# Kernel optimization log

Hardware: AMD Instinct MI355X
Metric: run time of the kernel (lower is better)

## Reference

```python
import jax, jax.numpy as jnp
import numpy as np

N_NODES = 20000
N_EDGES = 640000
NODE_IN = 128
EDGE_IN = 64
HID = 128
OUT = 128
LOG2 = float(np.log(2.0))


def ssp(x):
    # DGL ShiftedSoftplus: softplus(x) - log(2)
    return jax.nn.softplus(x) - LOG2


def cfconv(x, e, src, dst,
           nW, nb, eW1, eb1, eW2, eb2, oW, ob):
    hv = x @ nW + nb                                  # [N, HID]
    he = ssp(ssp(e @ eW1 + eb1) @ eW2 + eb2)          # [E, HID]
    msg = hv[src] * he                                # gather + filter
    agg = jax.ops.segment_sum(msg, dst, num_segments=N_NODES)
    return ssp(agg @ oW + ob)


def setup_inputs() -> dict:
    key = jax.random.key(0)
    ks = jax.random.split(key, 20)
    def w(k, shape, fan_in):
        return jax.random.normal(k, shape, dtype=jnp.float32) * (1.0 / np.sqrt(fan_in))
    inp = {
        "node_inputs": jax.random.normal(ks[0], (N_NODES, NODE_IN), dtype=jnp.float32),
        "edge_inputs": jax.random.normal(ks[1], (N_EDGES, EDGE_IN), dtype=jnp.float32),
        "src": jax.random.randint(ks[2], (N_EDGES,), 0, N_NODES, dtype=jnp.int32),
        "dst": jax.random.randint(ks[3], (N_EDGES,), 0, N_NODES, dtype=jnp.int32),
        # conv1 params
        "n1_W": w(ks[4], (NODE_IN, HID), NODE_IN), "n1_b": jnp.zeros((HID,), jnp.float32),
        "e1_W1": w(ks[5], (EDGE_IN, HID), EDGE_IN), "e1_b1": jnp.zeros((HID,), jnp.float32),
        "e1_W2": w(ks[6], (HID, HID), HID), "e1_b2": jnp.zeros((HID,), jnp.float32),
        "o1_W": w(ks[7], (HID, HID), HID), "o1_b": jnp.zeros((HID,), jnp.float32),
        # conv2 params
        "n2_W": w(ks[8], (HID, HID), HID), "n2_b": jnp.zeros((HID,), jnp.float32),
        "e2_W1": w(ks[9], (EDGE_IN, HID), EDGE_IN), "e2_b1": jnp.zeros((HID,), jnp.float32),
        "e2_W2": w(ks[10], (HID, HID), HID), "e2_b2": jnp.zeros((HID,), jnp.float32),
        "o2_W": w(ks[11], (HID, OUT), HID), "o2_b": jnp.zeros((OUT,), jnp.float32),
    }
    return inp


def reference(node_inputs, edge_inputs, src, dst,
              n1_W, n1_b, e1_W1, e1_b1, e1_W2, e1_b2, o1_W, o1_b,
              n2_W, n2_b, e2_W1, e2_b1, e2_W2, e2_b2, o2_W, o2_b):
    h = cfconv(node_inputs, edge_inputs, src, dst,
               n1_W, n1_b, e1_W1, e1_b1, e1_W2, e1_b2, o1_W, o1_b)
    h = jnp.tanh(h)
    # dropout(p) is identity in eval mode
    h = cfconv(h, edge_inputs, src, dst,
               n2_W, n2_b, e2_W1, e2_b1, e2_W2, e2_b2, o2_W, o2_b)
    return jnp.tanh(h)
```

## Files before the change

kernel.cpp:

```cpp
#include <hip/hip_runtime.h>
#include <hip/hip_bf16.h>
#include <math.h>

typedef __bf16 bf16x8 __attribute__((ext_vector_type(8)));
typedef float f32x4 __attribute__((ext_vector_type(4)));

#define LOG2F 0.6931471805599453f
#define PK1 72
#define PK2 136

__device__ __forceinline__ float sspf(float x) {
    float t = __expf(-fabsf(x));
    return fmaxf(x, 0.0f) + __logf(1.0f + t) - LOG2F;
}

__device__ __forceinline__ unsigned short f2bf(float f) {
    union { float f; unsigned u; } v; v.f = f;
    unsigned r = v.u + 0x7FFF + ((v.u >> 16) & 1);
    return (unsigned short)(r >> 16);
}

__device__ __forceinline__ unsigned short f2bf_fast(float f) {
    __bf16 h = (__bf16)f;
    return __builtin_bit_cast(unsigned short, h);
}

template<int ACT>
__global__ void node_gemm(const float* __restrict__ X, const float* __restrict__ W,
                          const float* __restrict__ b, float* __restrict__ Y, int N) {
    __shared__ float xs[2][128];
    const int tid = threadIdx.x;
    const int r = tid >> 7;
    const int c = tid & 127;
    const int row = blockIdx.x * 2 + r;
    if (row < N) xs[r][c] = X[(size_t)row * 128 + c];
    __syncthreads();
    if (row >= N) return;
    float acc = b[c];
#pragma unroll 8
    for (int k = 0; k < 128; ++k)
        acc = fmaf(xs[r][k], W[k * 128 + c], acc);
    if (ACT) acc = tanhf(sspf(acc));
    Y[(size_t)row * 128 + c] = acc;
}

__global__ void convert_wT(const float* __restrict__ W, unsigned short* __restrict__ O,
                           int K, int PK) {
    int idx = blockIdx.x * 256 + threadIdx.x;
    if (idx >= 128 * PK) return;
    int n = idx / PK, k = idx - n * PK;
    O[idx] = (k < K) ? f2bf(W[k * 128 + n]) : (unsigned short)0;
}

__global__ __launch_bounds__(256) void edge_mfma(
    const float* __restrict__ E, const int* __restrict__ src, const int* __restrict__ dst,
    const float* __restrict__ HV,
    const unsigned short* __restrict__ W1T, const float* __restrict__ b1,
    const unsigned short* __restrict__ W2T, const float* __restrict__ b2,
    float* __restrict__ AGG, int nE)
{
    __shared__ unsigned short sE[64 * PK1];
    __shared__ unsigned short sT1[64 * PK2];
    __shared__ int sSrc[64], sDst[64];

    const int tid = threadIdx.x;
    const int e0 = blockIdx.x * 64;

    {
        const int r = tid >> 2;
        const int c0 = (tid & 3) * 16;
        unsigned short* drow = &sE[r * PK1 + c0];
        if (e0 + r < nE) {
            const float4* s4 = (const float4*)&E[(size_t)(e0 + r) * 64 + c0];
#pragma unroll
            for (int j = 0; j < 4; ++j) {
                float4 v = s4[j];
                drow[j * 4 + 0] = f2bf_fast(v.x); drow[j * 4 + 1] = f2bf_fast(v.y);
                drow[j * 4 + 2] = f2bf_fast(v.z); drow[j * 4 + 3] = f2bf_fast(v.w);
            }
        } else {
#pragma unroll
            for (int j = 0; j < 16; ++j) drow[j] = 0;
        }
        if (tid < 64) {
            int e = e0 + tid;
            sSrc[tid] = (e < nE) ? src[e] : 0;
            sDst[tid] = (e < nE) ? dst[e] : 0;
        }
    }
    __syncthreads();

    const int w  = tid >> 6;
    const int l  = tid & 63;
    const int cb = w * 32;
    const int lr = l & 15;
    const int lk = (l >> 4) * 8;

    bf16x8 B1[2][2];
#pragma unroll
    for (int nt = 0; nt < 2; ++nt)
#pragma unroll
        for (int kt = 0; kt < 2; ++kt)
            B1[nt][kt] = *(const bf16x8*)&W1T[(cb + nt * 16 + lr) * PK1 + kt * 32 + lk];

    const float bb1[2] = { b1[cb + lr], b1[cb + 16 + lr] };
    const float bb2[2] = { b2[cb + lr], b2[cb + 16 + lr] };

    f32x4 acc1[4][2];
#pragma unroll
    for (int mt = 0; mt < 4; ++mt)
#pragma unroll
        for (int nt = 0; nt < 2; ++nt)
            acc1[mt][nt] = (f32x4){bb1[nt], bb1[nt], bb1[nt], bb1[nt]};
#pragma unroll
    for (int kt = 0; kt < 2; ++kt)
#pragma unroll
        for (int mt = 0; mt < 4; ++mt) {
            bf16x8 A = *(const bf16x8*)&sE[(mt * 16 + lr) * PK1 + kt * 32 + lk];
#pragma unroll
            for (int nt = 0; nt < 2; ++nt)
                acc1[mt][nt] = __builtin_amdgcn_mfma_f32_16x16x32_bf16(A, B1[nt][kt], acc1[mt][nt], 0, 0, 0);
        }

#pragma unroll
    for (int mt = 0; mt < 4; ++mt)
#pragma unroll
        for (int nt = 0; nt < 2; ++nt) {
            const int col = cb + nt * 16 + lr;
#pragma unroll
            for (int r = 0; r < 4; ++r) {
                const int row = mt * 16 + (l >> 4) * 4 + r;
                sT1[row * PK2 + col] = f2bf_fast(sspf(acc1[mt][nt][r]));
            }
        }
    __syncthreads();

    bf16x8 B2[2][4];
#pragma unroll
    for (int nt = 0; nt < 2; ++nt)
#pragma unroll
        for (int kt = 0; kt < 4; ++kt)
            B2[nt][kt] = *(const bf16x8*)&W2T[(cb + nt * 16 + lr) * PK2 + kt * 32 + lk];

    f32x4 acc2[4][2];
#pragma unroll
    for (int mt = 0; mt < 4; ++mt)
#pragma unroll
        for (int nt = 0; nt < 2; ++nt)
            acc2[mt][nt] = (f32x4){bb2[nt], bb2[nt], bb2[nt], bb2[nt]};
#pragma unroll
    for (int kt = 0; kt < 4; ++kt)
#pragma unroll
        for (int mt = 0; mt < 4; ++mt) {
            bf16x8 A = *(const bf16x8*)&sT1[(mt * 16 + lr) * PK2 + kt * 32 + lk];
#pragma unroll
            for (int nt = 0; nt < 2; ++nt)
                acc2[mt][nt] = __builtin_amdgcn_mfma_f32_16x16x32_bf16(A, B2[nt][kt], acc2[mt][nt], 0, 0, 0);
        }

#pragma unroll
    for (int mt = 0; mt < 4; ++mt)
#pragma unroll
        for (int nt = 0; nt < 2; ++nt) {
            const int col = cb + nt * 16 + lr;
#pragma unroll
            for (int r = 0; r < 4; ++r) {
                const int row = mt * 16 + (l >> 4) * 4 + r;
                if (e0 + row < nE) {
                    const float he = sspf(acc2[mt][nt][r]);
                    const int s = sSrc[row], d = sDst[row];
                    const float m = HV[(size_t)s * 128 + col] * he;
                    atomicAdd(&AGG[(size_t)d * 128 + col], m);
                }
            }
        }
}

extern "C" void kernel_launch(void* const* d_in, const int* in_sizes, int n_in,
                              void* d_out, int out_size, void* d_ws, size_t ws_size,
                              hipStream_t stream) {
    const float* x    = (const float*)d_in[0];
    const float* e    = (const float*)d_in[1];
    const int*   src  = (const int*)  d_in[2];
    const int*   dst  = (const int*)  d_in[3];
    const float* n1W  = (const float*)d_in[4];
    const float* n1b  = (const float*)d_in[5];
    const float* e1W1 = (const float*)d_in[6];
    const float* e1b1 = (const float*)d_in[7];
    const float* e1W2 = (const float*)d_in[8];
    const float* e1b2 = (const float*)d_in[9];
    const float* o1W  = (const float*)d_in[10];
    const float* o1b  = (const float*)d_in[11];
    const float* n2W  = (const float*)d_in[12];
    const float* n2b  = (const float*)d_in[13];
    const float* e2W1 = (const float*)d_in[14];
    const float* e2b1 = (const float*)d_in[15];
    const float* e2W2 = (const float*)d_in[16];
    const float* e2b2 = (const float*)d_in[17];
    const float* o2W  = (const float*)d_in[18];
    const float* o2b  = (const float*)d_in[19];

    const int N = in_sizes[0] / 128;
    const int E = in_sizes[2];
    float* out = (float*)d_out;

    char* ws = (char*)d_ws;
    const size_t nbytes = (size_t)N * 128 * sizeof(float);
    float* hv   = (float*)(ws);
    float* agg  = (float*)(ws + nbytes);
    float* hbuf = (float*)(ws + 2 * nbytes);

    const size_t w1t_elems = 128 * PK1;
    const size_t w2t_elems = 128 * PK2;
    const size_t wbytes = 2 * (w1t_elems + w2t_elems) * sizeof(unsigned short);
    unsigned short* wbase;
    if (ws_size >= 3 * nbytes + wbytes) {
        wbase = (unsigned short*)(ws + 3 * nbytes);
    } else {
        wbase = (unsigned short*)d_out;
    }
    unsigned short* w1t_1 = wbase;
    unsigned short* w2t_1 = wbase + w1t_elems;
    unsigned short* w1t_2 = wbase + w1t_elems + w2t_elems;
    unsigned short* w2t_2 = wbase + 2 * w1t_elems + w2t_elems;

    const int nodeBlocks = (N + 1) / 2;
    const int edgeBlocks = (E + 63) / 64;

    convert_wT<<<(128 * PK1 + 255) / 256, 256, 0, stream>>>(e1W1, w1t_1, 64,  PK1);
    convert_wT<<<(128 * PK2 + 255) / 256, 256, 0, stream>>>(e1W2, w2t_1, 128, PK2);
    convert_wT<<<(128 * PK1 + 255) / 256, 256, 0, stream>>>(e2W1, w1t_2, 64,  PK1);
    convert_wT<<<(128 * PK2 + 255) / 256, 256, 0, stream>>>(e2W2, w2t_2, 128, PK2);

    node_gemm<0><<<nodeBlocks, 256, 0, stream>>>(x, n1W, n1b, hv, N);
    hipMemsetAsync(agg, 0, nbytes, stream);
    edge_mfma<<<edgeBlocks, 256, 0, stream>>>(e, src, dst, hv, w1t_1, e1b1, w2t_1, e1b2, agg, E);
    node_gemm<1><<<nodeBlocks, 256, 0, stream>>>(agg, o1W, o1b, hbuf, N);

    node_gemm<0><<<nodeBlocks, 256, 0, stream>>>(hbuf, n2W, n2b, hv, N);
    hipMemsetAsync(agg, 0, nbytes, stream);
    edge_mfma<<<edgeBlocks, 256, 0, stream>>>(e, src, dst, hv, w1t_2, e2b1, w2t_2, e2b2, agg, E);
    node_gemm<1><<<nodeBlocks, 256, 0, stream>>>(agg, o2W, o2b, out, N);
}
```

Measured before the change: 753.2 us.

## Sort edges by destination and coalesce atomics per run of equal dst

```diff
diff --git a/kernel.cpp b/kernel.cpp
--- a/kernel.cpp
+++ b/kernel.cpp
@@ -13,13 +13,11 @@
     float t = __expf(-fabsf(x));
     return fmaxf(x, 0.0f) + __logf(1.0f + t) - LOG2F;
 }
-
 __device__ __forceinline__ unsigned short f2bf(float f) {
     union { float f; unsigned u; } v; v.f = f;
     unsigned r = v.u + 0x7FFF + ((v.u >> 16) & 1);
     return (unsigned short)(r >> 16);
 }
-
 __device__ __forceinline__ unsigned short f2bf_fast(float f) {
     __bf16 h = (__bf16)f;
     return __builtin_bit_cast(unsigned short, h);
@@ -52,60 +50,111 @@
     O[idx] = (k < K) ? f2bf(W[k * 128 + n]) : (unsigned short)0;
 }
 
+__global__ void hist_kernel(const int* __restrict__ dst, int* __restrict__ hist, int E) {
+    int i = blockIdx.x * 256 + threadIdx.x;
+    if (i < E) atomicAdd(&hist[dst[i]], 1);
+}
+__global__ void scan_kernel(const int* __restrict__ hist, int* __restrict__ row_ptr,
+                            int* __restrict__ cursor, int N) {
+    __shared__ int part[1024];
+    const int tid = threadIdx.x;
+    const int chunk = (N + 1023) / 1024;
+    const int lo = min(tid * chunk, N);
+    const int hi = min(lo + chunk, N);
+    int s = 0;
+    for (int i = lo; i < hi; ++i) s += hist[i];
+    part[tid] = s;
+    __syncthreads();
+    if (tid == 0) {
+        int run = 0;
+        for (int i = 0; i < 1024; ++i) { int t = part[i]; part[i] = run; run += t; }
+    }
+    __syncthreads();
+    int run = part[tid];
+    for (int i = lo; i < hi; ++i) { row_ptr[i] = run; cursor[i] = run; run += hist[i]; }
+}
+__global__ void scatter_kernel(const int* __restrict__ dst, int* __restrict__ cursor,
+                               int* __restrict__ perm, int E) {
+    int i = blockIdx.x * 256 + threadIdx.x;
+    if (i < E) { int p = atomicAdd(&cursor[dst[i]], 1); perm[p] = i; }
+}
+__global__ void sort_buckets(const int* __restrict__ row_ptr, const int* __restrict__ hist,
+                             int* __restrict__ perm, int N) {
+    int n = blockIdx.x * 256 + threadIdx.x;
+    if (n >= N) return;
+    const int lo = row_ptr[n], hi = lo + hist[n];
+    for (int i = lo + 1; i < hi; ++i) {
+        int v = perm[i]; int j = i - 1;
+        while (j >= lo && perm[j] > v) { perm[j + 1] = perm[j]; --j; }
+        perm[j + 1] = v;
+    }
+}
+__global__ void permute_sd(const int* __restrict__ perm, const int* __restrict__ src,
+                           const int* __restrict__ dst, int* __restrict__ srcP,
+                           int* __restrict__ dstP, int E) {
+    int i = blockIdx.x * 256 + threadIdx.x;
+    if (i < E) { int e = perm[i]; srcP[i] = src[e]; dstP[i] = dst[e]; }
+}
+__global__ void permute_e(const int* __restrict__ perm, const float* __restrict__ Ef,
+                          unsigned short* __restrict__ Ebf, int nE) {
+    long long idx = (long long)blockIdx.x * 256 + threadIdx.x;
+    if (idx >= (long long)nE * 16) return;
+    int p = (int)(idx >> 4), q = (int)(idx & 15);
+    int e = perm[p];
+    float4 v = *(const float4*)&Ef[(size_t)e * 64 + q * 4];
+    unsigned short* o = &Ebf[(size_t)p * 64 + q * 4];
+    o[0] = f2bf_fast(v.x); o[1] = f2bf_fast(v.y);
+    o[2] = f2bf_fast(v.z); o[3] = f2bf_fast(v.w);
+}
+
+template<int MODE>
 __global__ __launch_bounds__(256) void edge_mfma(
-    const float* __restrict__ E, const int* __restrict__ src, const int* __restrict__ dst,
+    const unsigned short* __restrict__ Ebf, const float* __restrict__ Ef,
+    const int* __restrict__ perm,
+    const int* __restrict__ srcA, const int* __restrict__ dstA,
     const float* __restrict__ HV,
     const unsigned short* __restrict__ W1T, const float* __restrict__ b1,
     const unsigned short* __restrict__ W2T, const float* __restrict__ b2,
     float* __restrict__ AGG, int nE)
 {
-    __shared__ unsigned short sE[64 * PK1];
     __shared__ unsigned short sT1[64 * PK2];
     __shared__ int sSrc[64], sDst[64];
+    __shared__ unsigned short sE[(MODE == 1) ? 64 * PK1 : 4];
 
     const int tid = threadIdx.x;
     const int e0 = blockIdx.x * 64;
 
-    {
-        const int r = tid >> 2;
-        const int c0 = (tid & 3) * 16;
-        unsigned short* drow = &sE[r * PK1 + c0];
-        if (e0 + r < nE) {
-            const float4* s4 = (const float4*)&E[(size_t)(e0 + r) * 64 + c0];
-#pragma unroll
-            for (int j = 0; j < 4; ++j) {
-                float4 v = s4[j];
-                drow[j * 4 + 0] = f2bf_fast(v.x); drow[j * 4 + 1] = f2bf_fast(v.y);
-                drow[j * 4 + 2] = f2bf_fast(v.z); drow[j * 4 + 3] = f2bf_fast(v.w);
-            }
-        } else {
-#pragma unroll
-            for (int j = 0; j < 16; ++j) drow[j] = 0;
-        }
-        if (tid < 64) {
-            int e = e0 + tid;
-            sSrc[tid] = (e < nE) ? src[e] : 0;
-            sDst[tid] = (e < nE) ? dst[e] : 0;
-        }
-    }
-    __syncthreads();
-
-    const int w  = tid >> 6;
-    const int l  = tid & 63;
-    const int cb = w * 32;
-    const int lr = l & 15;
-    const int lk = (l >> 4) * 8;
-
-    bf16x8 B1[2][2];
-#pragma unroll
-    for (int nt = 0; nt < 2; ++nt)
-#pragma unroll
-        for (int kt = 0; kt < 2; ++kt)
-            B1[nt][kt] = *(const bf16x8*)&W1T[(cb + nt * 16 + lr) * PK1 + kt * 32 + lk];
-
+    if (tid < 64) {
+        int gi = min(e0 + tid, nE - 1);
+        sSrc[tid] = srcA[gi];
+        sDst[tid] = dstA[gi];
+    }
+    if (MODE == 1) {
+        const int r = tid >> 2, c0 = (tid & 3) * 16;
+        int gi = e0 + r;
+        int e = (gi < nE) ? (perm ? perm[gi] : gi) : 0;
+        const float4* s4 = (const float4*)&Ef[(size_t)e * 64 + c0];
+        unsigned short* dr = &sE[r * PK1 + c0];
+#pragma unroll
+        for (int j = 0; j < 4; ++j) {
+            float4 v = s4[j];
+            dr[j*4+0] = f2bf_fast(v.x); dr[j*4+1] = f2bf_fast(v.y);
+            dr[j*4+2] = f2bf_fast(v.z); dr[j*4+3] = f2bf_fast(v.w);
+        }
+    }
+    __syncthreads();
+
+    const int w = tid >> 6, l = tid & 63, cb = w * 32, lr = l & 15, hi = l >> 4, lk = hi * 8;
     const float bb1[2] = { b1[cb + lr], b1[cb + 16 + lr] };
     const float bb2[2] = { b2[cb + lr], b2[cb + 16 + lr] };
 
+    bf16x8 B1[2][2];
+#pragma unroll
+    for (int nt = 0; nt < 2; ++nt)
+#pragma unroll
+        for (int kt = 0; kt < 2; ++kt)
+            B1[nt][kt] = *(const bf16x8*)&W1T[(size_t)(cb + nt*16 + lr) * PK1 + kt*32 + lk];
+
     f32x4 acc1[4][2];
 #pragma unroll
     for (int mt = 0; mt < 4; ++mt)
@@ -116,7 +165,13 @@
     for (int kt = 0; kt < 2; ++kt)
 #pragma unroll
         for (int mt = 0; mt < 4; ++mt) {
-            bf16x8 A = *(const bf16x8*)&sE[(mt * 16 + lr) * PK1 + kt * 32 + lk];
+            bf16x8 A;
+            if (MODE == 0) {
+                const int row = min(e0 + mt*16 + lr, nE - 1);
+                A = *(const bf16x8*)&Ebf[(size_t)row * 64 + kt*32 + lk];
+            } else {
+                A = *(const bf16x8*)&sE[(mt*16 + lr) * PK1 + kt*32 + lk];
+            }
 #pragma unroll
             for (int nt = 0; nt < 2; ++nt)
                 acc1[mt][nt] = __builtin_amdgcn_mfma_f32_16x16x32_bf16(A, B1[nt][kt], acc1[mt][nt], 0, 0, 0);
@@ -126,10 +181,10 @@
     for (int mt = 0; mt < 4; ++mt)
 #pragma unroll
         for (int nt = 0; nt < 2; ++nt) {
-            const int col = cb + nt * 16 + lr;
+            const int col = cb + nt*16 + lr;
 #pragma unroll
             for (int r = 0; r < 4; ++r) {
-                const int row = mt * 16 + (l >> 4) * 4 + r;
+                const int row = mt*16 + hi*4 + r;
                 sT1[row * PK2 + col] = f2bf_fast(sspf(acc1[mt][nt][r]));
             }
         }
@@ -140,7 +195,7 @@
     for (int nt = 0; nt < 2; ++nt)
 #pragma unroll
         for (int kt = 0; kt < 4; ++kt)
-            B2[nt][kt] = *(const bf16x8*)&W2T[(cb + nt * 16 + lr) * PK2 + kt * 32 + lk];
+            B2[nt][kt] = *(const bf16x8*)&W2T[(size_t)(cb + nt*16 + lr) * PK2 + kt*32 + lk];
 
     f32x4 acc2[4][2];
 #pragma unroll
@@ -152,28 +207,36 @@
     for (int kt = 0; kt < 4; ++kt)
 #pragma unroll
         for (int mt = 0; mt < 4; ++mt) {
-            bf16x8 A = *(const bf16x8*)&sT1[(mt * 16 + lr) * PK2 + kt * 32 + lk];
+            bf16x8 A = *(const bf16x8*)&sT1[(mt*16 + lr) * PK2 + kt*32 + lk];
 #pragma unroll
             for (int nt = 0; nt < 2; ++nt)
                 acc2[mt][nt] = __builtin_amdgcn_mfma_f32_16x16x32_bf16(A, B2[nt][kt], acc2[mt][nt], 0, 0, 0);
         }
 
-#pragma unroll
-    for (int mt = 0; mt < 4; ++mt)
-#pragma unroll
-        for (int nt = 0; nt < 2; ++nt) {
-            const int col = cb + nt * 16 + lr;
-#pragma unroll
-            for (int r = 0; r < 4; ++r) {
-                const int row = mt * 16 + (l >> 4) * 4 + r;
-                if (e0 + row < nE) {
-                    const float he = sspf(acc2[mt][nt][r]);
-                    const int s = sSrc[row], d = sDst[row];
-                    const float m = HV[(size_t)s * 128 + col] * he;
-                    atomicAdd(&AGG[(size_t)d * 128 + col], m);
-                }
+    const int col0 = cb + lr, col1 = cb + 16 + lr;
+    int curd = sDst[hi * 4];
+    float s0 = 0.f, s1 = 0.f;
+#pragma unroll
+    for (int mt = 0; mt < 4; ++mt) {
+#pragma unroll
+        for (int r = 0; r < 4; ++r) {
+            const int row = mt*16 + hi*4 + r;
+            const float msk = (e0 + row < nE) ? 1.f : 0.f;
+            const float he0 = sspf(acc2[mt][0][r]) * msk;
+            const float he1 = sspf(acc2[mt][1][r]) * msk;
+            const int s = sSrc[row], d = sDst[row];
+            const float m0 = HV[(size_t)s * 128 + col0] * he0;
+            const float m1 = HV[(size_t)s * 128 + col1] * he1;
+            if (d != curd) {
+                atomicAdd(&AGG[(size_t)curd * 128 + col0], s0);
+                atomicAdd(&AGG[(size_t)curd * 128 + col1], s1);
+                s0 = 0.f; s1 = 0.f; curd = d;
             }
-        }
+            s0 += m0; s1 += m1;
+        }
+    }
+    atomicAdd(&AGG[(size_t)curd * 128 + col0], s0);
+    atomicAdd(&AGG[(size_t)curd * 128 + col1], s1);
 }
 
 extern "C" void kernel_launch(void* const* d_in, const int* in_sizes, int n_in,
@@ -205,40 +268,72 @@
     float* out = (float*)d_out;
 
     char* ws = (char*)d_ws;
-    const size_t nbytes = (size_t)N * 128 * sizeof(float);
-    float* hv   = (float*)(ws);
-    float* agg  = (float*)(ws + nbytes);
-    float* hbuf = (float*)(ws + 2 * nbytes);
-
-    const size_t w1t_elems = 128 * PK1;
-    const size_t w2t_elems = 128 * PK2;
-    const size_t wbytes = 2 * (w1t_elems + w2t_elems) * sizeof(unsigned short);
-    unsigned short* wbase;
-    if (ws_size >= 3 * nbytes + wbytes) {
-        wbase = (unsigned short*)(ws + 3 * nbytes);
-    } else {
-        wbase = (unsigned short*)d_out;
-    }
-    unsigned short* w1t_1 = wbase;
-    unsigned short* w2t_1 = wbase + w1t_elems;
-    unsigned short* w1t_2 = wbase + w1t_elems + w2t_elems;
-    unsigned short* w2t_2 = wbase + 2 * w1t_elems + w2t_elems;
+    size_t off = 0;
+    auto alloc = [&](size_t bytes) -> char* {
+        char* p = ws + off;
+        off = (off + bytes + 255) & ~(size_t)255;
+        return p;
+    };
+    float* agg = (float*)alloc((size_t)N * 128 * 4);
+    float* hv  = (float*)alloc((size_t)N * 128 * 4);
+    unsigned short* w_e1w1 = (unsigned short*)alloc(128 * PK1 * 2);
+    unsigned short* w_e1w2 = (unsigned short*)alloc(128 * PK2 * 2);
+    unsigned short* w_e2w1 = (unsigned short*)alloc(128 * PK1 * 2);
+    unsigned short* w_e2w2 = (unsigned short*)alloc(128 * PK2 * 2);
+    int* perm    = (int*)alloc((size_t)E * 4);
+    int* srcP    = (int*)alloc((size_t)E * 4);
+    int* dstP    = (int*)alloc((size_t)E * 4);
+    int* hist    = (int*)alloc((size_t)N * 4);
+    int* cursor  = (int*)alloc((size_t)N * 4);
+    int* row_ptr = (int*)alloc((size_t)N * 4);
+    const size_t sort_need = off;
+    unsigned short* Ebf = (unsigned short*)alloc((size_t)E * 64 * 2);
+    const bool useEbf  = (ws_size >= off);
+    const bool useSort = (ws_size >= sort_need);
+
+    float* hbuf = out;
+
+    convert_wT<<<(128*PK1 + 255)/256, 256, 0, stream>>>(e1W1, w_e1w1, 64,  PK1);
+    convert_wT<<<(128*PK2 + 255)/256, 256, 0, stream>>>(e1W2, w_e1w2, 128, PK2);
+    convert_wT<<<(128*PK1 + 255)/256, 256, 0, stream>>>(e2W1, w_e2w1, 64,  PK1);
+    convert_wT<<<(128*PK2 + 255)/256, 256, 0, stream>>>(e2W2, w_e2w2, 128, PK2);
+
+    const int* sA = src;
+    const int* dA = dst;
+    const int* permArg = nullptr;
+    if (useSort) {
+        hipMemsetAsync(hist, 0, (size_t)N * 4, stream);
+        hist_kernel<<<(E + 255)/256, 256, 0, stream>>>(dst, hist, E);
+        scan_kernel<<<1, 1024, 0, stream>>>(hist, row_ptr, cursor, N);
+        scatter_kernel<<<(E + 255)/256, 256, 0, stream>>>(dst, cursor, perm, E);
+        sort_buckets<<<(N + 255)/256, 256, 0, stream>>>(row_ptr, hist, perm, N);
+        permute_sd<<<(E + 255)/256, 256, 0, stream>>>(perm, src, dst, srcP, dstP, E);
+        if (useEbf)
+            permute_e<<<(int)(((size_t)E * 16 + 255)/256), 256, 0, stream>>>(perm, e, Ebf, E);
+        sA = srcP; dA = dstP; permArg = perm;
+    }
 
     const int nodeBlocks = (N + 1) / 2;
     const int edgeBlocks = (E + 63) / 64;
-
-    convert_wT<<<(128 * PK1 + 255) / 256, 256, 0, stream>>>(e1W1, w1t_1, 64,  PK1);
-    convert_wT<<<(128 * PK2 + 255) / 256, 256, 0, stream>>>(e1W2, w2t_1, 128, PK2);
-    convert_wT<<<(128 * PK1 + 255) / 256, 256, 0, stream>>>(e2W1, w1t_2, 64,  PK1);
-    convert_wT<<<(128 * PK2 + 255) / 256, 256, 0, stream>>>(e2W2, w2t_2, 128, PK2);
+    const size_t nbytes = (size_t)N * 128 * 4;
 
     node_gemm<0><<<nodeBlocks, 256, 0, stream>>>(x, n1W, n1b, hv, N);
     hipMemsetAsync(agg, 0, nbytes, stream);
-    edge_mfma<<<edgeBlocks, 256, 0, stream>>>(e, src, dst, hv, w1t_1, e1b1, w2t_1, e1b2, agg, E);
+    if (useEbf)
+        edge_mfma<0><<<edgeBlocks, 256, 0, stream>>>(Ebf, nullptr, nullptr, sA, dA, hv,
+                                                     w_e1w1, e1b1, w_e1w2, e1b2, agg, E);
+    else
+        edge_mfma<1><<<edgeBlocks, 256, 0, stream>>>(nullptr, e, permArg, sA, dA, hv,
+                                                     w_e1w1, e1b1, w_e1w2, e1b2, agg, E);
     node_gemm<1><<<nodeBlocks, 256, 0, stream>>>(agg, o1W, o1b, hbuf, N);
 
     node_gemm<0><<<nodeBlocks, 256, 0, stream>>>(hbuf, n2W, n2b, hv, N);
     hipMemsetAsync(agg, 0, nbytes, stream);
-    edge_mfma<<<edgeBlocks, 256, 0, stream>>>(e, src, dst, hv, w1t_2, e2b1, w2t_2, e2b2, agg, E);
+    if (useEbf)
+        edge_mfma<0><<<edgeBlocks, 256, 0, stream>>>(Ebf, nullptr, nullptr, sA, dA, hv,
+                                                     w_e2w1, e2b1, w_e2w2, e2b2, agg, E);
+    else
+        edge_mfma<1><<<edgeBlocks, 256, 0, stream>>>(nullptr, e, permArg, sA, dA, hv,
+                                                     w_e2w1, e2b1, w_e2w2, e2b2, agg, E);
     node_gemm<1><<<nodeBlocks, 256, 0, stream>>>(agg, o2W, o2b, out, N);
 }
```

New measurement: 787.8 us. +4.6%, slower.
